# Performance work log

Hardware: AMD Instinct MI355X
Metric: run time of the kernel (lower is better)

The kernel has to match this reference:

```python
import jax, jax.numpy as jnp
import numpy as np

N_NODES = 10000
N_GRAPHS = 64
NEG_SLOPE = 0.2
EPS = 1e-16


def gat_conv(x, src, dst, W, a_src, a_dst, bias, heads, out_ch, num_nodes):
    """PyG GATConv (shared lin, add_self_loops already applied to src/dst)."""
    xl = (x @ W).reshape(num_nodes, heads, out_ch)          # [N,H,C]
    alpha_s = jnp.einsum('nhc,hc->nh', xl, a_src)           # [N,H]
    alpha_d = jnp.einsum('nhc,hc->nh', xl, a_dst)           # [N,H]
    e = jax.nn.leaky_relu(alpha_s[src] + alpha_d[dst], NEG_SLOPE)  # [E,H]
    # segment softmax over incoming edges of each destination node
    emax = jax.ops.segment_max(e, dst, num_segments=num_nodes)
    emax = jnp.where(jnp.isfinite(emax), emax, 0.0)
    ee = jnp.exp(e - emax[dst])
    denom = jax.ops.segment_sum(ee, dst, num_segments=num_nodes)
    alpha = ee / (denom[dst] + EPS)                         # [E,H]
    msg = xl[src] * alpha[:, :, None]                       # [E,H,C]
    out = jax.ops.segment_sum(msg, dst, num_segments=num_nodes)  # [N,H,C]
    return out.reshape(num_nodes, heads * out_ch) + bias


def setup_inputs() -> dict:
    key = jax.random.key(0)
    ks = jax.random.split(key, 16)
    H, C, IN = 8, 128, 128
    x = jax.random.normal(ks[0], (N_NODES, IN), jnp.float32)
    edge_index = jax.random.randint(ks[1], (2, 320000), 0, N_NODES, jnp.int64)
    batch = jnp.sort(jax.random.randint(ks[2], (N_NODES,), 0, N_GRAPHS, jnp.int64))
    g = lambda k, shp, fan: jax.random.normal(k, shp, jnp.float32) * (1.0 / np.sqrt(fan))
    return {
        'x': x, 'edge_index': edge_index, 'batch': batch,
        'W1': g(ks[3], (IN, H * C), IN),
        'a_src1': g(ks[4], (H, C), C), 'a_dst1': g(ks[5], (H, C), C),
        'b1': jnp.zeros((H * C,), jnp.float32),
        'W2': g(ks[6], (H * C, C), H * C),
        'a_src2': g(ks[7], (1, C), C), 'a_dst2': g(ks[8], (1, C), C),
        'b2': jnp.zeros((C,), jnp.float32),
        'lin1_w': g(ks[9], (C, 128), C), 'lin1_b': jnp.zeros((128,), jnp.float32),
        'lin2_w': g(ks[10], (128, 1), 128), 'lin2_b': jnp.zeros((1,), jnp.float32),
    }


def reference(x, edge_index, batch, W1, a_src1, a_dst1, b1, W2, a_src2, a_dst2, b2,
              lin1_w, lin1_b, lin2_w, lin2_b):
    loops = jnp.arange(N_NODES, dtype=edge_index.dtype)
    src = jnp.concatenate([edge_index[0], loops])
    dst = jnp.concatenate([edge_index[1], loops])
    h = jax.nn.elu(gat_conv(x, src, dst, W1, a_src1, a_dst1, b1, 8, 128, N_NODES))
    h = jax.nn.elu(gat_conv(h, src, dst, W2, a_src2, a_dst2, b2, 1, 128, N_NODES))
    # global mean pool over graphs
    sums = jax.ops.segment_sum(h, batch, num_segments=N_GRAPHS)
    cnts = jax.ops.segment_sum(jnp.ones((N_NODES,), h.dtype), batch, num_segments=N_GRAPHS)
    pooled = sums / jnp.maximum(cnts, 1.0)[:, None]         # [G,128]
    z = jax.nn.relu(pooled @ lin1_w + lin1_b)
    return (z @ lin2_w + lin2_b).squeeze(1)                 # [G]
```

## Files before the change

### kernel.cpp

```cpp
#include <hip/hip_runtime.h>
#include <math.h>

#define N_NODES 10000
#define N_GRAPHS 64
#define E_RAW 320000
#define E_ALL (E_RAW + N_NODES)
#define NEG_SLOPE 0.2f
#define EPS 1e-16f
#define CAP 192

typedef unsigned short ushort_t;
typedef short short8 __attribute__((ext_vector_type(8)));
typedef float floatx4 __attribute__((ext_vector_type(4)));

static __device__ __forceinline__ float bfl(unsigned u) {
  union { unsigned u; float f; } v; v.u = u << 16; return v.f;
}
static __device__ __forceinline__ float bfh(unsigned u) {
  union { unsigned u; float f; } v; v.u = u & 0xFFFF0000u; return v.f;
}
static __device__ __forceinline__ ushort_t f2bf(float f) {
  union { float f; unsigned u; } v; v.f = f;
  unsigned r = v.u + 0x7FFFu + ((v.u >> 16) & 1u);
  return (ushort_t)(r >> 16);
}

static __device__ __forceinline__ void load16_lds(const ushort_t* gp, ushort_t* ldsbase, int lane) {
#if __has_builtin(__builtin_amdgcn_global_load_lds)
  __builtin_amdgcn_global_load_lds((const __attribute__((address_space(1))) void*)gp,
                                   (__attribute__((address_space(3))) void*)ldsbase, 16, 0, 0);
#else
  *(uint4*)(ldsbase + lane * 8) = *(const uint4*)gp;
#endif
}

static __device__ __forceinline__ void swz_one(const float* __restrict__ W,
                                               ushort_t* __restrict__ Wsw,
                                               int idx, int K, int N) {
  int NT = N >> 4;
  int lane = idx & 63, tile = idx >> 6;
  int nt = tile % NT, kt = tile / NT;
  int n = nt * 16 + (lane & 15);
  int kb = kt * 32 + (lane >> 4) * 8;
  ushort4 lo, hi;
  lo.x = f2bf(W[(size_t)(kb + 0) * N + n]); lo.y = f2bf(W[(size_t)(kb + 1) * N + n]);
  lo.z = f2bf(W[(size_t)(kb + 2) * N + n]); lo.w = f2bf(W[(size_t)(kb + 3) * N + n]);
  hi.x = f2bf(W[(size_t)(kb + 4) * N + n]); hi.y = f2bf(W[(size_t)(kb + 5) * N + n]);
  hi.z = f2bf(W[(size_t)(kb + 6) * N + n]); hi.w = f2bf(W[(size_t)(kb + 7) * N + n]);
  *(ushort4*)(Wsw + (size_t)idx * 8) = lo;
  *(ushort4*)(Wsw + (size_t)idx * 8 + 4) = hi;
}

__global__ __launch_bounds__(1024) void prep_k(const float* __restrict__ x,
                                               const int* __restrict__ batch,
                                               const float* __restrict__ W1,
                                               const float* __restrict__ W2,
                                               ushort_t* __restrict__ xb,
                                               ushort_t* __restrict__ W1sw,
                                               ushort_t* __restrict__ W2sw,
                                               float* __restrict__ zero0,
                                               int* __restrict__ poolcnt) {
  __shared__ int shm[N_GRAPHS];
  const int b = blockIdx.x, t = threadIdx.x;
  if (b < 49) {
    int i4 = b * 1024 + t;
    if (i4 < 49548) *(float4*)(zero0 + i4 * 4) = make_float4(0.f, 0.f, 0.f, 0.f);
  } else if (b == 49) {
    if (t < N_GRAPHS) shm[t] = 0;
    __syncthreads();
    for (int n = t; n < N_NODES; n += 1024) atomicAdd(&shm[batch[n]], 1);
    __syncthreads();
    if (t < N_GRAPHS) poolcnt[t] = shm[t];
  } else if (b < 363) {
    int i4 = (b - 50) * 1024 + t;
    if (i4 < 320000) {
      float4 v = *(const float4*)(x + (size_t)i4 * 4);
      ushort4 o;
      o.x = f2bf(v.x); o.y = f2bf(v.y); o.z = f2bf(v.z); o.w = f2bf(v.w);
      *(ushort4*)(xb + (size_t)i4 * 4) = o;
    }
  } else if (b < 379) {
    int idx = (b - 363) * 1024 + t;
    if (idx < 16384) swz_one(W1, W1sw, idx, 128, 1024);
  } else {
    int idx = (b - 379) * 1024 + t;
    if (idx < 16384) swz_one(W2, W2sw, idx, 1024, 128);
  }
}

__global__ __launch_bounds__(256) void g1f_k(const ushort_t* __restrict__ A,
                                             const ushort_t* __restrict__ Bsw,
                                             ushort_t* __restrict__ Cb,
                                             const float* __restrict__ aS,
                                             const float* __restrict__ aD,
                                             float* __restrict__ asO,
                                             float* __restrict__ adO,
                                             const int* __restrict__ ei,
                                             int* __restrict__ degc,
                                             int* __restrict__ csr) {
  __shared__ ushort_t Albuf[32 * 512];
  __shared__ float epi[4][16][68];
  const int bid = blockIdx.x, t = threadIdx.x;
  if (bid >= 632) {
    int e = (bid - 632) * 256 + t;
    if (e < E_ALL) {
      int s, d;
      if (e < E_RAW) { s = ei[e]; d = ei[E_RAW + e]; }
      else           { s = d = e - E_RAW; }
      int pos = atomicAdd(&degc[d], 1);
      if (pos < CAP) csr[d * CAP + pos] = s;
    }
    return;
  }
  const int M = N_NODES, K = 128, NT = 64;
  const int lane = t & 63, w = t >> 6;
  const int wm = w >> 1, wn = w & 1;
  const int m0 = (bid >> 3) * 128;
  const int n0 = (bid & 7) * 128;
  const int g = lane >> 4, l16 = lane & 15;

  #pragma unroll
  for (int i = 0; i < 8; i++) {
    int tile = w * 8 + i;
    int mtl = tile >> 2, kt = tile & 3;
    int r = m0 + mtl * 16 + l16; r = r < M ? r : M - 1;
    load16_lds(A + (size_t)r * K + kt * 32 + g * 8, &Albuf[tile * 512], lane);
  }
  __syncthreads();

  floatx4 acc[4][4] = {};
  #pragma unroll
  for (int kt = 0; kt < 4; kt++) {
    short8 a[4], b[4];
    #pragma unroll
    for (int mi = 0; mi < 4; mi++)
      a[mi] = *(const short8*)&Albuf[(((wm * 4 + mi) * 4 + kt) * 64 + lane) * 8];
    #pragma unroll
    for (int ni = 0; ni < 4; ni++) {
      int nt = (n0 >> 4) + wn * 4 + ni;
      b[ni] = *(const short8*)(Bsw + ((size_t)(kt * NT + nt) * 64 + lane) * 8);
    }
    #pragma unroll
    for (int mi = 0; mi < 4; mi++)
      #pragma unroll
      for (int ni = 0; ni < 4; ni++)
        acc[mi][ni] = __builtin_amdgcn_mfma_f32_16x16x32_bf16(a[mi], b[ni], acc[mi][ni], 0, 0, 0);
  }

  const int h = bid & 7;
  const int r = lane >> 2, c0 = (lane & 3) * 16;
  const int colh = wn * 64 + c0;
  float asc[16], adc[16];
  #pragma unroll
  for (int c = 0; c < 16; c++) { asc[c] = aS[h * 128 + colh + c]; adc[c] = aD[h * 128 + colh + c]; }
  #pragma unroll
  for (int mi = 0; mi < 4; mi++) {
    #pragma unroll
    for (int ni = 0; ni < 4; ni++)
      #pragma unroll
      for (int reg = 0; reg < 4; reg++)
        epi[w][g * 4 + reg][ni * 16 + l16] = acc[mi][ni][reg];
    float4 v0 = *(float4*)&epi[w][r][c0];
    float4 v1 = *(float4*)&epi[w][r][c0 + 4];
    float4 v2 = *(float4*)&epi[w][r][c0 + 8];
    float4 v3 = *(float4*)&epi[w][r][c0 + 12];
    float vr[16] = {v0.x,v0.y,v0.z,v0.w, v1.x,v1.y,v1.z,v1.w,
                    v2.x,v2.y,v2.z,v2.w, v3.x,v3.y,v3.z,v3.w};
    int grow = m0 + wm * 64 + mi * 16 + r;
    float sp = 0.f, dp = 0.f;
    ushort_t hv[16];
    #pragma unroll
    for (int c = 0; c < 16; c++) {
      sp = fmaf(vr[c], asc[c], sp);
      dp = fmaf(vr[c], adc[c], dp);
      hv[c] = f2bf(vr[c]);
    }
    sp += __shfl_xor(sp, 1); sp += __shfl_xor(sp, 2);
    dp += __shfl_xor(dp, 1); dp += __shfl_xor(dp, 2);
    if (grow < M) {
      uint4 u0, u1;
      u0.x = (unsigned)hv[0] | ((unsigned)hv[1] << 16);
      u0.y = (unsigned)hv[2] | ((unsigned)hv[3] << 16);
      u0.z = (unsigned)hv[4] | ((unsigned)hv[5] << 16);
      u0.w = (unsigned)hv[6] | ((unsigned)hv[7] << 16);
      u1.x = (unsigned)hv[8] | ((unsigned)hv[9] << 16);
      u1.y = (unsigned)hv[10] | ((unsigned)hv[11] << 16);
      u1.z = (unsigned)hv[12] | ((unsigned)hv[13] << 16);
      u1.w = (unsigned)hv[14] | ((unsigned)hv[15] << 16);
      ushort_t* cp = Cb + (size_t)grow * 1024 + (bid & 7) * 128 + wn * 64 + c0;
      *(uint4*)cp = u0;
      *(uint4*)(cp + 8) = u1;
      if ((lane & 3) == 0) {
        atomicAdd(&asO[grow * 8 + h], sp);
        atomicAdd(&adO[grow * 8 + h], dp);
      }
    }
  }
}

__global__ __launch_bounds__(256) void gemm2_k(const ushort_t* __restrict__ A,
                                               const ushort_t* __restrict__ Bsw,
                                               ushort_t* __restrict__ Cb,
                                               const float* __restrict__ aS,
                                               const float* __restrict__ aD,
                                               float* __restrict__ asO,
                                               float* __restrict__ adO) {
  const int M = N_NODES, K = 1024, NT = 8;
  __shared__ ushort_t Albuf[4 * 512];
  __shared__ float epi[4][16][36];
  const int t = threadIdx.x, lane = t & 63, w = t >> 6;
  const int mb0 = blockIdx.x * 16;
  const int g = lane >> 4, l16 = lane & 15;

  floatx4 acc[2] = {};
  for (int ch = 0; ch < 8; ch++) {
    {
      int r = mb0 + l16; r = r < M ? r : M - 1;
      load16_lds(A + (size_t)r * K + (ch * 4 + w) * 32 + g * 8, &Albuf[w * 512], lane);
    }
    __syncthreads();
    #pragma unroll
    for (int ks = 0; ks < 4; ks++) {
      short8 a = *(const short8*)&Albuf[(ks * 64 + lane) * 8];
      #pragma unroll
      for (int ni = 0; ni < 2; ni++) {
        int nt = w * 2 + ni, ktg = ch * 4 + ks;
        short8 b = *(const short8*)(Bsw + ((size_t)(ktg * NT + nt) * 64 + lane) * 8);
        acc[ni] = __builtin_amdgcn_mfma_f32_16x16x32_bf16(a, b, acc[ni], 0, 0, 0);
      }
    }
    __syncthreads();
  }

  const int r = lane >> 2, c0 = (lane & 3) * 8;
  const int colh = w * 32 + c0;
  float asc[8], adc[8];
  #pragma unroll
  for (int c = 0; c < 8; c++) { asc[c] = aS[colh + c]; adc[c] = aD[colh + c]; }
  #pragma unroll
  for (int ni = 0; ni < 2; ni++)
    #pragma unroll
    for (int reg = 0; reg < 4; reg++)
      epi[w][g * 4 + reg][ni * 16 + l16] = acc[ni][reg];
  float4 v0 = *(float4*)&epi[w][r][c0];
  float4 v1 = *(float4*)&epi[w][r][c0 + 4];
  float vr[8] = {v0.x, v0.y, v0.z, v0.w, v1.x, v1.y, v1.z, v1.w};
  int grow = mb0 + r;
  float sp = 0.f, dp = 0.f;
  ushort_t hv[8];
  #pragma unroll
  for (int c = 0; c < 8; c++) {
    sp = fmaf(vr[c], asc[c], sp);
    dp = fmaf(vr[c], adc[c], dp);
    hv[c] = f2bf(vr[c]);
  }
  sp += __shfl_xor(sp, 1); sp += __shfl_xor(sp, 2);
  dp += __shfl_xor(dp, 1); dp += __shfl_xor(dp, 2);
  if (grow < M) {
    uint4 u0;
    u0.x = (unsigned)hv[0] | ((unsigned)hv[1] << 16);
    u0.y = (unsigned)hv[2] | ((unsigned)hv[3] << 16);
    u0.z = (unsigned)hv[4] | ((unsigned)hv[5] << 16);
    u0.w = (unsigned)hv[6] | ((unsigned)hv[7] << 16);
    *(uint4*)(Cb + (size_t)grow * 128 + colh) = u0;
    if ((lane & 3) == 0) {
      atomicAdd(&asO[grow], sp);
      atomicAdd(&adO[grow], dp);
    }
  }
}

__global__ __launch_bounds__(64) void agg1_k(const ushort_t* __restrict__ xlb,
                                             const float* __restrict__ as1,
                                             const float* __restrict__ ad1,
                                             const float* __restrict__ b1,
                                             const int* __restrict__ degc,
                                             const int* __restrict__ csr,
                                             ushort_t* __restrict__ out) {
  const int bid = blockIdx.x, t = threadIdx.x;
  const int h = bid & 7, dst = bid >> 3;
  int deg = degc[dst]; deg = deg < CAP ? deg : CAP;
  const int beg = dst * CAP;
  const int degp = (deg + 7) & ~7;
  __shared__ uint2 pr[CAP];
  float adh = ad1[dst * 8 + h];
  if (deg <= 64) {
    bool act = t < deg;
    int s = act ? csr[beg + t] : 0;
    float lg = -1e30f;
    if (act) {
      float v = as1[s * 8 + h] + adh;
      lg = v > 0.f ? v : NEG_SLOPE * v;
    }
    float pm = lg;
    #pragma unroll
    for (int off = 32; off; off >>= 1) pm = fmaxf(pm, __shfl_xor(pm, off));
    float ex = act ? __expf(lg - pm) : 0.f;
    float ps = ex;
    #pragma unroll
    for (int off = 32; off; off >>= 1) ps += __shfl_xor(ps, off);
    float inv = 1.0f / (ps + EPS);
    if (t < degp) pr[t] = act ? make_uint2((unsigned)(s * 2048), __float_as_uint(ex * inv))
                              : make_uint2(0u, 0u);
    __syncthreads();
  } else {
    __shared__ int ssg[CAP];
    __shared__ float alg[CAP];
    for (int e = t; e < deg; e += 64) ssg[e] = csr[beg + e];
    __syncthreads();
    float pm = -1e30f;
    for (int e = t; e < deg; e += 64) {
      float v = as1[ssg[e] * 8 + h] + adh;
      v = v > 0.f ? v : NEG_SLOPE * v;
      alg[e] = v;
      pm = fmaxf(pm, v);
    }
    #pragma unroll
    for (int off = 32; off; off >>= 1) pm = fmaxf(pm, __shfl_xor(pm, off));
    __syncthreads();
    float ps = 0.f;
    for (int e = t; e < deg; e += 64) ps += __expf(alg[e] - pm);
    #pragma unroll
    for (int off = 32; off; off >>= 1) ps += __shfl_xor(ps, off);
    float inv = 1.0f / (ps + EPS);
    for (int e = t; e < deg; e += 64)
      pr[e] = make_uint2((unsigned)(ssg[e] * 2048), __float_as_uint(__expf(alg[e] - pm) * inv));
    for (int e = deg + t; e < degp; e += 64) pr[e] = make_uint2(0u, 0u);
    __syncthreads();
  }
  const char* xbase = (const char*)xlb;
  const unsigned toff = (unsigned)(h * 256 + 4 * t);
  float accA[4] = {}, accB[4] = {};
  for (int e0 = 0; e0 < degp; e0 += 8) {
    #pragma unroll
    for (int j = 0; j < 8; j++) {
      uint2 p = pr[e0 + j];
      unsigned u = *(const unsigned*)(xbase + (p.x + toff));
      float a = __uint_as_float(p.y);
      accA[j & 3] = fmaf(a, bfl(u), accA[j & 3]);
      accB[j & 3] = fmaf(a, bfh(u), accB[j & 3]);
    }
  }
  float acc0 = (accA[0] + accA[1]) + (accA[2] + accA[3]);
  float acc1 = (accB[0] + accB[1]) + (accB[2] + accB[3]);
  int o = h * 128 + 2 * t;
  float v0 = acc0 + b1[o];
  float v1 = acc1 + b1[o + 1];
  v0 = v0 > 0.f ? v0 : (__expf(v0) - 1.0f);
  v1 = v1 > 0.f ? v1 : (__expf(v1) - 1.0f);
  unsigned up = (unsigned)f2bf(v0) | ((unsigned)f2bf(v1) << 16);
  *(unsigned*)(out + (size_t)dst * 1024 + o) = up;
}

__global__ __launch_bounds__(64) void agg2_k(const ushort_t* __restrict__ xlb2,
                                             const float* __restrict__ as2,
                                             const float* __restrict__ ad2,
                                             const float* __restrict__ b2,
                                             const int* __restrict__ degc,
                                             const int* __restrict__ csr,
                                             const int* __restrict__ batch,
                                             float* __restrict__ poolsum) {
  int dst = blockIdx.x, t = threadIdx.x;
  int deg = degc[dst]; deg = deg < CAP ? deg : CAP;
  int beg = dst * CAP;
  const int degp = (deg + 7) & ~7;
  float adv = ad2[dst];
  __shared__ uint2 pr[CAP];
  if (deg <= 64) {
    bool act = t < deg;
    int s = act ? csr[beg + t] : 0;
    float lg = -1e30f;
    if (act) {
      float v = as2[s] + adv;
      lg = v > 0.f ? v : NEG_SLOPE * v;
    }
    float pm = lg;
    #pragma unroll
    for (int off = 32; off; off >>= 1) pm = fmaxf(pm, __shfl_xor(pm, off));
    float ex = act ? __expf(lg - pm) : 0.f;
    float ps = ex;
    #pragma unroll
    for (int off = 32; off; off >>= 1) ps += __shfl_xor(ps, off);
    float inv = 1.0f / (ps + EPS);
    if (t < degp) pr[t] = act ? make_uint2((unsigned)(s * 256), __float_as_uint(ex * inv))
                              : make_uint2(0u, 0u);
    __syncthreads();
  } else {
    __shared__ int ssg[CAP];
    __shared__ float alg[CAP];
    for (int e = t; e < deg; e += 64) ssg[e] = csr[beg + e];
    __syncthreads();
    float pm = -1e30f;
    for (int e = t; e < deg; e += 64) {
      float v = as2[ssg[e]] + adv;
      v = v > 0.f ? v : NEG_SLOPE * v;
      alg[e] = v;
      pm = fmaxf(pm, v);
    }
    #pragma unroll
    for (int off = 32; off; off >>= 1) pm = fmaxf(pm, __shfl_xor(pm, off));
    __syncthreads();
    float ps = 0.f;
    for (int e = t; e < deg; e += 64) ps += __expf(alg[e] - pm);
    #pragma unroll
    for (int off = 32; off; off >>= 1) ps += __shfl_xor(ps, off);
    float inv = 1.0f / (ps + EPS);
    for (int e = t; e < deg; e += 64)
      pr[e] = make_uint2((unsigned)(ssg[e] * 256), __float_as_uint(__expf(alg[e] - pm) * inv));
    for (int e = deg + t; e < degp; e += 64) pr[e] = make_uint2(0u, 0u);
    __syncthreads();
  }
  const char* xbase = (const char*)xlb2;
  const unsigned toff = (unsigned)(4 * t);
  float accA[4] = {}, accB[4] = {};
  for (int e0 = 0; e0 < degp; e0 += 8) {
    #pragma unroll
    for (int j = 0; j < 8; j++) {
      uint2 p = pr[e0 + j];
      unsigned u = *(const unsigned*)(xbase + (p.x + toff));
      float a = __uint_as_float(p.y);
      accA[j & 3] = fmaf(a, bfl(u), accA[j & 3]);
      accB[j & 3] = fmaf(a, bfh(u), accB[j & 3]);
    }
  }
  float acc0 = (accA[0] + accA[1]) + (accA[2] + accA[3]);
  float acc1 = (accB[0] + accB[1]) + (accB[2] + accB[3]);
  int c0 = 2 * t;
  float v0 = acc0 + b2[c0];
  float v1 = acc1 + b2[c0 + 1];
  v0 = v0 > 0.f ? v0 : (__expf(v0) - 1.0f);
  v1 = v1 > 0.f ? v1 : (__expf(v1) - 1.0f);
  int g = batch[dst];
  atomicAdd(&poolsum[g * 128 + c0], v0);
  atomicAdd(&poolsum[g * 128 + c0 + 1], v1);
}

__global__ __launch_bounds__(128) void final_k(const float* __restrict__ poolsum,
                                               const int* __restrict__ cnt,
                                               const float* __restrict__ l1w,
                                               const float* __restrict__ l1b,
                                               const float* __restrict__ l2w,
                                               const float* __restrict__ l2b,
                                               float* __restrict__ out) {
  int g = blockIdx.x, t = threadIdx.x;
  __shared__ float pooled[128];
  float c = fmaxf((float)cnt[g], 1.0f);
  pooled[t] = poolsum[g * 128 + t] / c;
  __syncthreads();
  float acc = l1b[t];
  for (int i = 0; i < 128; i++) acc = fmaf(pooled[i], l1w[i * 128 + t], acc);
  acc = fmaxf(acc, 0.0f);
  float p = acc * l2w[t];
  #pragma unroll
  for (int off = 32; off; off >>= 1) p += __shfl_down(p, off);
  __shared__ float r[2];
  if ((t & 63) == 0) r[t >> 6] = p;
  __syncthreads();
  if (t == 0) out[g] = r[0] + r[1] + l2b[0];
}

extern "C" void kernel_launch(void* const* d_in, const int* in_sizes, int n_in,
                              void* d_out, int out_size, void* d_ws, size_t ws_size,
                              hipStream_t stream) {
  const float* x    = (const float*)d_in[0];
  const int*   ei   = (const int*)d_in[1];
  const int*   batch= (const int*)d_in[2];
  const float* W1   = (const float*)d_in[3];
  const float* aS1  = (const float*)d_in[4];
  const float* aD1  = (const float*)d_in[5];
  const float* b1   = (const float*)d_in[6];
  const float* W2   = (const float*)d_in[7];
  const float* aS2  = (const float*)d_in[8];
  const float* aD2  = (const float*)d_in[9];
  const float* b2   = (const float*)d_in[10];
  const float* l1w  = (const float*)d_in[11];
  const float* l1b  = (const float*)d_in[12];
  const float* l2w  = (const float*)d_in[13];
  const float* l2b  = (const float*)d_in[14];
  float* out = (float*)d_out;

  ushort_t* xlb1   = (ushort_t*)d_ws;
  ushort_t* h1b    = xlb1 + 10240000;
  ushort_t* xlb2   = h1b + 10240000;
  ushort_t* xb     = xlb2 + 1280000;
  ushort_t* W1sw   = xb + 1280000;
  ushort_t* W2sw   = W1sw + 131072;
  float*    zero0  = (float*)(W2sw + 131072);
  float*    as1    = zero0;
  float*    ad1    = as1 + 80000;
  float*    as2    = ad1 + 80000;
  float*    ad2    = as2 + 10000;
  float*    poolsum= ad2 + 10000;
  int*      degc   = (int*)(poolsum + 8192);
  int*      poolcnt= degc + 10000;
  int*      csr    = poolcnt + 64;

  prep_k<<<395, 1024, 0, stream>>>(x, batch, W1, W2, xb, W1sw, W2sw, zero0, poolcnt);
  g1f_k<<<632 + 1290, 256, 0, stream>>>(xb, W1sw, xlb1, aS1, aD1, as1, ad1, ei, degc, csr);
  agg1_k<<<N_NODES * 8, 64, 0, stream>>>(xlb1, as1, ad1, b1, degc, csr, h1b);
  gemm2_k<<<625, 256, 0, stream>>>(h1b, W2sw, xlb2, aS2, aD2, as2, ad2);
  agg2_k<<<N_NODES, 64, 0, stream>>>(xlb2, as2, ad2, b2, degc, csr, batch, poolsum);
  final_k<<<N_GRAPHS, 128, 0, stream>>>(poolsum, poolcnt, l1w, l1b, l2w, l2b, out);
}
```

Baseline: 209.9 us.

## Aggregate raw features before layer-1 GEMM using precomputed W·a attention vectors

Layer 1 is reordered so the attention-weighted neighbour sum runs over the 128-dim bf16 input rows per head, and the per-head GEMM is applied afterwards. Attention logits come from x times precomputed W1·a_src and W1·a_dst vectors, so the GEMM no longer needs atomic logit accumulation. Bias and ELU move into the GEMM epilogue. This cuts the gather traffic in the aggregation, which previously read 1024-wide projected rows per edge. In exchange the GEMM input is now an N×8×128 aggregated tensor, there is an extra small logit kernel, and rounding changes because the sum is taken before the projection.

```diff
diff --git a/kernel.cpp b/kernel.cpp
--- a/kernel.cpp
+++ b/kernel.cpp
@@ -55,54 +55,71 @@
                                                const int* __restrict__ batch,
                                                const float* __restrict__ W1,
                                                const float* __restrict__ W2,
+                                               const float* __restrict__ aS1,
+                                               const float* __restrict__ aD1,
                                                ushort_t* __restrict__ xb,
                                                ushort_t* __restrict__ W1sw,
                                                ushort_t* __restrict__ W2sw,
                                                float* __restrict__ zero0,
-                                               int* __restrict__ poolcnt) {
+                                               int* __restrict__ poolcnt,
+                                               float* __restrict__ wAs,
+                                               float* __restrict__ wAd) {
   __shared__ int shm[N_GRAPHS];
   const int b = blockIdx.x, t = threadIdx.x;
-  if (b < 49) {
+  if (b < 10) {
     int i4 = b * 1024 + t;
-    if (i4 < 49548) *(float4*)(zero0 + i4 * 4) = make_float4(0.f, 0.f, 0.f, 0.f);
-  } else if (b == 49) {
+    if (i4 < 9548) *(float4*)(zero0 + i4 * 4) = make_float4(0.f, 0.f, 0.f, 0.f);
+  } else if (b == 10) {
     if (t < N_GRAPHS) shm[t] = 0;
     __syncthreads();
     for (int n = t; n < N_NODES; n += 1024) atomicAdd(&shm[batch[n]], 1);
     __syncthreads();
     if (t < N_GRAPHS) poolcnt[t] = shm[t];
-  } else if (b < 363) {
-    int i4 = (b - 50) * 1024 + t;
+  } else if (b < 324) {
+    int i4 = (b - 11) * 1024 + t;
     if (i4 < 320000) {
       float4 v = *(const float4*)(x + (size_t)i4 * 4);
       ushort4 o;
       o.x = f2bf(v.x); o.y = f2bf(v.y); o.z = f2bf(v.z); o.w = f2bf(v.w);
       *(ushort4*)(xb + (size_t)i4 * 4) = o;
     }
-  } else if (b < 379) {
-    int idx = (b - 363) * 1024 + t;
+  } else if (b < 340) {
+    int idx = (b - 324) * 1024 + t;
     if (idx < 16384) swz_one(W1, W1sw, idx, 128, 1024);
+  } else if (b < 356) {
+    int idx = (b - 340) * 1024 + t;
+    if (idx < 16384) swz_one(W2, W2sw, idx, 1024, 128);
   } else {
-    int idx = (b - 379) * 1024 + t;
-    if (idx < 16384) swz_one(W2, W2sw, idx, 1024, 128);
-  }
-}
-
-__global__ __launch_bounds__(256) void g1f_k(const ushort_t* __restrict__ A,
-                                             const ushort_t* __restrict__ Bsw,
-                                             ushort_t* __restrict__ Cb,
-                                             const float* __restrict__ aS,
-                                             const float* __restrict__ aD,
-                                             float* __restrict__ asO,
-                                             float* __restrict__ adO,
-                                             const int* __restrict__ ei,
+    int h = t >> 7, k = t & 127;
+    const float* wrow = W1 + (size_t)k * 1024 + h * 128;
+    const float* as = aS1 + h * 128;
+    const float* ad = aD1 + h * 128;
+    float accS = 0.f, accD = 0.f;
+    for (int c = 0; c < 128; c += 4) {
+      float4 wv = *(const float4*)(wrow + c);
+      float4 sv = *(const float4*)(as + c);
+      float4 dv = *(const float4*)(ad + c);
+      accS = fmaf(wv.x, sv.x, accS); accS = fmaf(wv.y, sv.y, accS);
+      accS = fmaf(wv.z, sv.z, accS); accS = fmaf(wv.w, sv.w, accS);
+      accD = fmaf(wv.x, dv.x, accD); accD = fmaf(wv.y, dv.y, accD);
+      accD = fmaf(wv.z, dv.z, accD); accD = fmaf(wv.w, dv.w, accD);
+    }
+    wAs[h * 128 + k] = accS;
+    wAd[h * 128 + k] = accD;
+  }
+}
+
+__global__ __launch_bounds__(256) void lgf_k(const int* __restrict__ ei,
                                              int* __restrict__ degc,
-                                             int* __restrict__ csr) {
-  __shared__ ushort_t Albuf[32 * 512];
-  __shared__ float epi[4][16][68];
+                                             int* __restrict__ csr,
+                                             const float* __restrict__ x,
+                                             const float* __restrict__ wAs,
+                                             const float* __restrict__ wAd,
+                                             float* __restrict__ as1,
+                                             float* __restrict__ ad1) {
   const int bid = blockIdx.x, t = threadIdx.x;
-  if (bid >= 632) {
-    int e = (bid - 632) * 256 + t;
+  if (bid < 1290) {
+    int e = bid * 256 + t;
     if (e < E_ALL) {
       int s, d;
       if (e < E_RAW) { s = ei[e]; d = ei[E_RAW + e]; }
@@ -112,11 +129,129 @@
     }
     return;
   }
-  const int M = N_NODES, K = 128, NT = 64;
+  int nb = bid - 1290;
+  int n = nb * 16 + (t >> 4);
+  int cb = t & 15, h = cb >> 1, sd = cb & 1;
+  const float* w = (sd ? wAd : wAs) + h * 128;
+  const float* xr = x + (size_t)n * 128;
+  float acc = 0.f;
+  for (int k = 0; k < 128; k += 4) {
+    float4 xv = *(const float4*)(xr + k);
+    float4 wv = *(const float4*)(w + k);
+    acc = fmaf(xv.x, wv.x, acc); acc = fmaf(xv.y, wv.y, acc);
+    acc = fmaf(xv.z, wv.z, acc); acc = fmaf(xv.w, wv.w, acc);
+  }
+  if (sd) ad1[n * 8 + h] = acc;
+  else    as1[n * 8 + h] = acc;
+}
+
+__global__ __launch_bounds__(64) void agg1x_k(const ushort_t* __restrict__ xb,
+                                              const float* __restrict__ as1,
+                                              const float* __restrict__ ad1,
+                                              const int* __restrict__ degc,
+                                              const int* __restrict__ csr,
+                                              ushort_t* __restrict__ aggx) {
+  const int dst = blockIdx.x, t = threadIdx.x;
+  int deg = degc[dst]; deg = deg < CAP ? deg : CAP;
+  const int beg = dst * CAP;
+  __shared__ unsigned offs[CAP];
+  __shared__ float al[CAP][8];
+  float ad[8];
+  {
+    float4 d0 = *(const float4*)(ad1 + dst * 8);
+    float4 d1 = *(const float4*)(ad1 + dst * 8 + 4);
+    ad[0] = d0.x; ad[1] = d0.y; ad[2] = d0.z; ad[3] = d0.w;
+    ad[4] = d1.x; ad[5] = d1.y; ad[6] = d1.z; ad[7] = d1.w;
+  }
+  float pmax[8];
+  #pragma unroll
+  for (int h = 0; h < 8; h++) pmax[h] = -1e30f;
+  for (int e = t; e < deg; e += 64) {
+    int s = csr[beg + e];
+    offs[e] = (unsigned)(s * 256);
+    float4 a0 = *(const float4*)(as1 + s * 8);
+    float4 a1 = *(const float4*)(as1 + s * 8 + 4);
+    float lg[8] = {a0.x + ad[0], a0.y + ad[1], a0.z + ad[2], a0.w + ad[3],
+                   a1.x + ad[4], a1.y + ad[5], a1.z + ad[6], a1.w + ad[7]};
+    #pragma unroll
+    for (int h = 0; h < 8; h++) {
+      float v = lg[h]; v = v > 0.f ? v : NEG_SLOPE * v;
+      al[e][h] = v;
+      pmax[h] = fmaxf(pmax[h], v);
+    }
+  }
+  #pragma unroll
+  for (int h = 0; h < 8; h++) {
+    #pragma unroll
+    for (int off = 32; off; off >>= 1) pmax[h] = fmaxf(pmax[h], __shfl_xor(pmax[h], off));
+  }
+  float ps[8] = {};
+  for (int e = t; e < deg; e += 64) {
+    #pragma unroll
+    for (int h = 0; h < 8; h++) {
+      float ex = __expf(al[e][h] - pmax[h]);
+      al[e][h] = ex;
+      ps[h] += ex;
+    }
+  }
+  #pragma unroll
+  for (int h = 0; h < 8; h++) {
+    #pragma unroll
+    for (int off = 32; off; off >>= 1) ps[h] += __shfl_xor(ps[h], off);
+    ps[h] = 1.0f / (ps[h] + EPS);
+  }
+  for (int e = t; e < deg; e += 64) {
+    #pragma unroll
+    for (int h = 0; h < 8; h++) al[e][h] *= ps[h];
+  }
+  const int degp = (deg + 3) & ~3;
+  for (int e = deg + t; e < degp; e += 64) {
+    offs[e] = 0;
+    #pragma unroll
+    for (int h = 0; h < 8; h++) al[e][h] = 0.f;
+  }
+  __syncthreads();
+  const char* xbase = (const char*)xb;
+  const unsigned toff = (unsigned)(4 * t);
+  float aL[8] = {}, aH[8] = {};
+  for (int e0 = 0; e0 < degp; e0 += 4) {
+    #pragma unroll
+    for (int j = 0; j < 4; j++) {
+      int e = e0 + j;
+      unsigned u = *(const unsigned*)(xbase + (offs[e] + toff));
+      float4 q0 = *(const float4*)&al[e][0];
+      float4 q1 = *(const float4*)&al[e][4];
+      float lo = bfl(u), hi = bfh(u);
+      aL[0] = fmaf(q0.x, lo, aL[0]); aH[0] = fmaf(q0.x, hi, aH[0]);
+      aL[1] = fmaf(q0.y, lo, aL[1]); aH[1] = fmaf(q0.y, hi, aH[1]);
+      aL[2] = fmaf(q0.z, lo, aL[2]); aH[2] = fmaf(q0.z, hi, aH[2]);
+      aL[3] = fmaf(q0.w, lo, aL[3]); aH[3] = fmaf(q0.w, hi, aH[3]);
+      aL[4] = fmaf(q1.x, lo, aL[4]); aH[4] = fmaf(q1.x, hi, aH[4]);
+      aL[5] = fmaf(q1.y, lo, aL[5]); aH[5] = fmaf(q1.y, hi, aH[5]);
+      aL[6] = fmaf(q1.z, lo, aL[6]); aH[6] = fmaf(q1.z, hi, aH[6]);
+      aL[7] = fmaf(q1.w, lo, aL[7]); aH[7] = fmaf(q1.w, hi, aH[7]);
+    }
+  }
+  ushort_t* op = aggx + (size_t)dst * 1024 + 2 * t;
+  #pragma unroll
+  for (int h = 0; h < 8; h++) {
+    unsigned up = (unsigned)f2bf(aL[h]) | ((unsigned)f2bf(aH[h]) << 16);
+    *(unsigned*)(op + h * 128) = up;
+  }
+}
+
+__global__ __launch_bounds__(256) void gemm1h_k(const ushort_t* __restrict__ A,
+                                                const ushort_t* __restrict__ Bsw,
+                                                const float* __restrict__ b1,
+                                                ushort_t* __restrict__ Cb) {
+  __shared__ ushort_t Albuf[32 * 512];
+  __shared__ float epi[4][16][68];
+  const int bid = blockIdx.x, t = threadIdx.x;
+  const int M = N_NODES, NT = 64;
   const int lane = t & 63, w = t >> 6;
   const int wm = w >> 1, wn = w & 1;
   const int m0 = (bid >> 3) * 128;
-  const int n0 = (bid & 7) * 128;
+  const int h = bid & 7;
   const int g = lane >> 4, l16 = lane & 15;
 
   #pragma unroll
@@ -124,7 +259,7 @@
     int tile = w * 8 + i;
     int mtl = tile >> 2, kt = tile & 3;
     int r = m0 + mtl * 16 + l16; r = r < M ? r : M - 1;
-    load16_lds(A + (size_t)r * K + kt * 32 + g * 8, &Albuf[tile * 512], lane);
+    load16_lds(A + ((size_t)r * 8 + h) * 128 + kt * 32 + g * 8, &Albuf[tile * 512], lane);
   }
   __syncthreads();
 
@@ -137,7 +272,7 @@
       a[mi] = *(const short8*)&Albuf[(((wm * 4 + mi) * 4 + kt) * 64 + lane) * 8];
     #pragma unroll
     for (int ni = 0; ni < 4; ni++) {
-      int nt = (n0 >> 4) + wn * 4 + ni;
+      int nt = h * 8 + wn * 4 + ni;
       b[ni] = *(const short8*)(Bsw + ((size_t)(kt * NT + nt) * 64 + lane) * 8);
     }
     #pragma unroll
@@ -147,12 +282,11 @@
         acc[mi][ni] = __builtin_amdgcn_mfma_f32_16x16x32_bf16(a[mi], b[ni], acc[mi][ni], 0, 0, 0);
   }
 
-  const int h = bid & 7;
   const int r = lane >> 2, c0 = (lane & 3) * 16;
   const int colh = wn * 64 + c0;
-  float asc[16], adc[16];
-  #pragma unroll
-  for (int c = 0; c < 16; c++) { asc[c] = aS[h * 128 + colh + c]; adc[c] = aD[h * 128 + colh + c]; }
+  float bv[16];
+  #pragma unroll
+  for (int c = 0; c < 16; c++) bv[c] = b1[h * 128 + colh + c];
   #pragma unroll
   for (int mi = 0; mi < 4; mi++) {
     #pragma unroll
@@ -167,17 +301,14 @@
     float vr[16] = {v0.x,v0.y,v0.z,v0.w, v1.x,v1.y,v1.z,v1.w,
                     v2.x,v2.y,v2.z,v2.w, v3.x,v3.y,v3.z,v3.w};
     int grow = m0 + wm * 64 + mi * 16 + r;
-    float sp = 0.f, dp = 0.f;
-    ushort_t hv[16];
-    #pragma unroll
-    for (int c = 0; c < 16; c++) {
-      sp = fmaf(vr[c], asc[c], sp);
-      dp = fmaf(vr[c], adc[c], dp);
-      hv[c] = f2bf(vr[c]);
-    }
-    sp += __shfl_xor(sp, 1); sp += __shfl_xor(sp, 2);
-    dp += __shfl_xor(dp, 1); dp += __shfl_xor(dp, 2);
     if (grow < M) {
+      ushort_t hv[16];
+      #pragma unroll
+      for (int c = 0; c < 16; c++) {
+        float v = vr[c] + bv[c];
+        v = v > 0.f ? v : (__expf(v) - 1.0f);
+        hv[c] = f2bf(v);
+      }
       uint4 u0, u1;
       u0.x = (unsigned)hv[0] | ((unsigned)hv[1] << 16);
       u0.y = (unsigned)hv[2] | ((unsigned)hv[3] << 16);
@@ -187,13 +318,9 @@
       u1.y = (unsigned)hv[10] | ((unsigned)hv[11] << 16);
       u1.z = (unsigned)hv[12] | ((unsigned)hv[13] << 16);
       u1.w = (unsigned)hv[14] | ((unsigned)hv[15] << 16);
-      ushort_t* cp = Cb + (size_t)grow * 1024 + (bid & 7) * 128 + wn * 64 + c0;
+      ushort_t* cp = Cb + (size_t)grow * 1024 + h * 128 + colh;
       *(uint4*)cp = u0;
       *(uint4*)(cp + 8) = u1;
-      if ((lane & 3) == 0) {
-        atomicAdd(&asO[grow * 8 + h], sp);
-        atomicAdd(&adO[grow * 8 + h], dp);
-      }
     }
   }
 }
@@ -268,88 +395,6 @@
       atomicAdd(&adO[grow], dp);
     }
   }
-}
-
-__global__ __launch_bounds__(64) void agg1_k(const ushort_t* __restrict__ xlb,
-                                             const float* __restrict__ as1,
-                                             const float* __restrict__ ad1,
-                                             const float* __restrict__ b1,
-                                             const int* __restrict__ degc,
-                                             const int* __restrict__ csr,
-                                             ushort_t* __restrict__ out) {
-  const int bid = blockIdx.x, t = threadIdx.x;
-  const int h = bid & 7, dst = bid >> 3;
-  int deg = degc[dst]; deg = deg < CAP ? deg : CAP;
-  const int beg = dst * CAP;
-  const int degp = (deg + 7) & ~7;
-  __shared__ uint2 pr[CAP];
-  float adh = ad1[dst * 8 + h];
-  if (deg <= 64) {
-    bool act = t < deg;
-    int s = act ? csr[beg + t] : 0;
-    float lg = -1e30f;
-    if (act) {
-      float v = as1[s * 8 + h] + adh;
-      lg = v > 0.f ? v : NEG_SLOPE * v;
-    }
-    float pm = lg;
-    #pragma unroll
-    for (int off = 32; off; off >>= 1) pm = fmaxf(pm, __shfl_xor(pm, off));
-    float ex = act ? __expf(lg - pm) : 0.f;
-    float ps = ex;
-    #pragma unroll
-    for (int off = 32; off; off >>= 1) ps += __shfl_xor(ps, off);
-    float inv = 1.0f / (ps + EPS);
-    if (t < degp) pr[t] = act ? make_uint2((unsigned)(s * 2048), __float_as_uint(ex * inv))
-                              : make_uint2(0u, 0u);
-    __syncthreads();
-  } else {
-    __shared__ int ssg[CAP];
-    __shared__ float alg[CAP];
-    for (int e = t; e < deg; e += 64) ssg[e] = csr[beg + e];
-    __syncthreads();
-    float pm = -1e30f;
-    for (int e = t; e < deg; e += 64) {
-      float v = as1[ssg[e] * 8 + h] + adh;
-      v = v > 0.f ? v : NEG_SLOPE * v;
-      alg[e] = v;
-      pm = fmaxf(pm, v);
-    }
-    #pragma unroll
-    for (int off = 32; off; off >>= 1) pm = fmaxf(pm, __shfl_xor(pm, off));
-    __syncthreads();
-    float ps = 0.f;
-    for (int e = t; e < deg; e += 64) ps += __expf(alg[e] - pm);
-    #pragma unroll
-    for (int off = 32; off; off >>= 1) ps += __shfl_xor(ps, off);
-    float inv = 1.0f / (ps + EPS);
-    for (int e = t; e < deg; e += 64)
-      pr[e] = make_uint2((unsigned)(ssg[e] * 2048), __float_as_uint(__expf(alg[e] - pm) * inv));
-    for (int e = deg + t; e < degp; e += 64) pr[e] = make_uint2(0u, 0u);
-    __syncthreads();
-  }
-  const char* xbase = (const char*)xlb;
-  const unsigned toff = (unsigned)(h * 256 + 4 * t);
-  float accA[4] = {}, accB[4] = {};
-  for (int e0 = 0; e0 < degp; e0 += 8) {
-    #pragma unroll
-    for (int j = 0; j < 8; j++) {
-      uint2 p = pr[e0 + j];
-      unsigned u = *(const unsigned*)(xbase + (p.x + toff));
-      float a = __uint_as_float(p.y);
-      accA[j & 3] = fmaf(a, bfl(u), accA[j & 3]);
-      accB[j & 3] = fmaf(a, bfh(u), accB[j & 3]);
-    }
-  }
-  float acc0 = (accA[0] + accA[1]) + (accA[2] + accA[3]);
-  float acc1 = (accB[0] + accB[1]) + (accB[2] + accB[3]);
-  int o = h * 128 + 2 * t;
-  float v0 = acc0 + b1[o];
-  float v1 = acc1 + b1[o + 1];
-  v0 = v0 > 0.f ? v0 : (__expf(v0) - 1.0f);
-  v1 = v1 > 0.f ? v1 : (__expf(v1) - 1.0f);
-  unsigned up = (unsigned)f2bf(v0) | ((unsigned)f2bf(v1) << 16);
-  *(unsigned*)(out + (size_t)dst * 1024 + o) = up;
 }
 
 __global__ __launch_bounds__(64) void agg2_k(const ushort_t* __restrict__ xlb2,
@@ -479,25 +524,29 @@
   const float* l2b  = (const float*)d_in[14];
   float* out = (float*)d_out;
 
-  ushort_t* xlb1   = (ushort_t*)d_ws;
-  ushort_t* h1b    = xlb1 + 10240000;
+  ushort_t* xb     = (ushort_t*)d_ws;
+  ushort_t* aggx   = xb + 1280000;
+  ushort_t* h1b    = aggx + 10240000;
   ushort_t* xlb2   = h1b + 10240000;
-  ushort_t* xb     = xlb2 + 1280000;
-  ushort_t* W1sw   = xb + 1280000;
+  ushort_t* W1sw   = xlb2 + 1280000;
   ushort_t* W2sw   = W1sw + 131072;
-  float*    zero0  = (float*)(W2sw + 131072);
-  float*    as1    = zero0;
+  float*    wAs    = (float*)(W2sw + 131072);
+  float*    wAd    = wAs + 1024;
+  float*    as1    = wAd + 1024;
   float*    ad1    = as1 + 80000;
-  float*    as2    = ad1 + 80000;
+  float*    zero0  = ad1 + 80000;
+  float*    as2    = zero0;
   float*    ad2    = as2 + 10000;
   float*    poolsum= ad2 + 10000;
   int*      degc   = (int*)(poolsum + 8192);
-  int*      poolcnt= degc + 10000;
+  int*      poolcnt= (int*)(zero0 + 38192);
   int*      csr    = poolcnt + 64;
 
-  prep_k<<<395, 1024, 0, stream>>>(x, batch, W1, W2, xb, W1sw, W2sw, zero0, poolcnt);
-  g1f_k<<<632 + 1290, 256, 0, stream>>>(xb, W1sw, xlb1, aS1, aD1, as1, ad1, ei, degc, csr);
-  agg1_k<<<N_NODES * 8, 64, 0, stream>>>(xlb1, as1, ad1, b1, degc, csr, h1b);
+  prep_k<<<357, 1024, 0, stream>>>(x, batch, W1, W2, aS1, aD1, xb, W1sw, W2sw,
+                                   zero0, poolcnt, wAs, wAd);
+  lgf_k<<<1290 + 625, 256, 0, stream>>>(ei, degc, csr, x, wAs, wAd, as1, ad1);
+  agg1x_k<<<N_NODES, 64, 0, stream>>>(xb, as1, ad1, degc, csr, aggx);
+  gemm1h_k<<<632, 256, 0, stream>>>(aggx, W1sw, b1, h1b);
   gemm2_k<<<625, 256, 0, stream>>>(h1b, W2sw, xlb2, aS2, aD2, as2, ad2);
   agg2_k<<<N_NODES, 64, 0, stream>>>(xlb2, as2, ad2, b2, degc, csr, batch, poolsum);
   final_k<<<N_GRAPHS, 128, 0, stream>>>(poolsum, poolcnt, l1w, l1b, l2w, l2b, out);
```

New measurement: 222.9 us. 1.06x slower.
